# Kernel tuning notes

Measured on AMD Instinct MI355X. Metric: run time of the kernel, lower is better.

The kernel has to match this reference:

```python
import jax, jax.numpy as jnp
import numpy as np

N = 256   # num_atoms
V = 64    # v_dim
E = 64    # e_dim
S = 16    # num_sims
H = 16    # hidden size hard-coded in the module


def setup_inputs() -> dict:
    key = jax.random.key(0)
    ks = jax.random.split(key, 12)
    # edge index lists equivalent to the one-hot rel_rec / rel_send matmuls
    off_diag = np.ones((N, N), dtype=np.float32) - np.eye(N, dtype=np.float32)
    send_np, recv_np = np.where(off_diag)  # rows=senders ([0]), cols=receivers ([1])
    def w(k, shape):
        fan_in = shape[0]
        return (jax.random.normal(k, shape, jnp.float32) / np.sqrt(fan_in)).astype(jnp.float32)
    return {
        "t": jnp.zeros((), jnp.float32),
        "v0": jax.random.normal(ks[0], (S, N, V), jnp.float32),
        "e0": jax.random.normal(ks[1], (S, N, N - 1, E), jnp.float32),
        "wv1": w(ks[2], (E, H)), "bv1": jnp.zeros((H,), jnp.float32),
        "wv2": w(ks[3], (H, V)), "bv2": jnp.zeros((V,), jnp.float32),
        "we1": w(ks[4], (2 * V, H)), "be1": jnp.zeros((H,), jnp.float32),
        "we2": w(ks[5], (H, E)), "be2": jnp.zeros((E,), jnp.float32),
        "recv_idx": jnp.asarray(recv_np, jnp.int32),
        "send_idx": jnp.asarray(send_np, jnp.int32),
    }


def reference(t, v0, e0, wv1, bv1, wv2, bv2, we1, be1, we2, be2, recv_idx, send_idx):
    # dv = mlp_v(sum_j e0[:, :, j, :])  -> [S, N, V]
    ev = jnp.sum(e0, axis=2)                               # [S, N, E]
    dv = jnp.tanh(ev @ wv1 + bv1) @ wv2 + bv2              # [S, N, V]

    # node2edge: one-hot matmuls == gathers along the node axis
    receivers = v0[:, recv_idx, :]                          # [S, N*(N-1), V]
    senders = v0[:, send_idx, :]                            # [S, N*(N-1), V]
    edges = jnp.concatenate([receivers, senders], axis=-1)  # [S, N*(N-1), 2V]

    de = jnp.tanh(edges @ we1 + be1) @ we2 + be2            # [S, N*(N-1), E]
    de = de.reshape(de.shape[0], N, N - 1, de.shape[-1])    # [S, N, N-1, E]
    return (dv, de)
```

## Files before the change

### kernel.cpp

```cpp
#include <hip/hip_runtime.h>
#include <cstddef>

#define NN 256
#define VD 64
#define ED 64
#define SD 16
#define HD 16
#define EPS 65280

__device__ __forceinline__ float fast_tanh(float x) {
    float e = __expf(2.0f * x);
    float r = __builtin_amdgcn_rcpf(e + 1.0f);
    return 1.0f - 2.0f * r;
}

__global__ __launch_bounds__(256) void precompute_ab(
    const float* __restrict__ v0, const float* __restrict__ we1,
    float* __restrict__ a_tab, float* __restrict__ b_tab) {
    int t = threadIdx.x;
    int i = t & 15;
    int nl = t >> 4;
    int node = blockIdx.x * 16 + nl;
    const float* vrow = v0 + (size_t)node * VD;
    float a = 0.f, b = 0.f;
    #pragma unroll
    for (int k = 0; k < VD; ++k) {
        float x = vrow[k];
        a += x * we1[k * HD + i];
        b += x * we1[(VD + k) * HD + i];
    }
    a_tab[node * HD + i] = a;
    b_tab[node * HD + i] = b;
}

__global__ __launch_bounds__(256) void dv_kernel(
    const float* __restrict__ e0,
    const float* __restrict__ wv1, const float* __restrict__ bv1,
    const float* __restrict__ wv2, const float* __restrict__ bv2,
    float* __restrict__ dv_out) {
    __shared__ float red[1024];
    __shared__ float ev_s[64];
    __shared__ float h_s[16];
    int t = threadIdx.x;
    int node = blockIdx.x;
    const float* base = e0 + (size_t)node * 255 * ED;
    int c = t & 15;
    int g = t >> 4;
    float4 acc = make_float4(0.f, 0.f, 0.f, 0.f);
    for (int j = g; j < 255; j += 16) {
        const float4 v = *(const float4*)(base + (size_t)j * ED + c * 4);
        acc.x += v.x; acc.y += v.y; acc.z += v.z; acc.w += v.w;
    }
    *(float4*)(red + g * 64 + c * 4) = acc;
    __syncthreads();
    if (t < 64) {
        float s = 0.f;
        #pragma unroll
        for (int gg = 0; gg < 16; ++gg) s += red[gg * 64 + t];
        ev_s[t] = s;
    }
    __syncthreads();
    if (t < 16) {
        float ah = bv1[t];
        #pragma unroll
        for (int e = 0; e < 64; ++e) ah += ev_s[e] * wv1[e * HD + t];
        h_s[t] = fast_tanh(ah);
    }
    __syncthreads();
    if (t < 64) {
        float o = bv2[t];
        #pragma unroll
        for (int i = 0; i < HD; ++i) o += h_s[i] * wv2[i * VD + t];
        dv_out[(size_t)node * VD + t] = o;
    }
}

__global__ __launch_bounds__(256) void de_kernel(
    const float* __restrict__ a_tab, const float* __restrict__ b_tab,
    const float* __restrict__ we2, const float* __restrict__ be1,
    const float* __restrict__ be2,
    const int* __restrict__ recv_idx, const int* __restrict__ send_idx,
    float* __restrict__ de_out) {
    __shared__ float h_s[64 * 20];
    int t = threadIdx.x;
    int s = blockIdx.y;
    int tile = blockIdx.x;
    int p = t & 63;
    int iq = t >> 6;
    int eg = tile * 64 + p;

    int r  = recv_idx[eg];
    int sd = send_idx[eg];
    const float4 av = *(const float4*)(a_tab + ((s << 8) + r)  * HD + iq * 4);
    const float4 bv = *(const float4*)(b_tab + ((s << 8) + sd) * HD + iq * 4);
    const float4 b1 = *(const float4*)(be1 + iq * 4);
    float4 hv;
    hv.x = fast_tanh(av.x + bv.x + b1.x);
    hv.y = fast_tanh(av.y + bv.y + b1.y);
    hv.z = fast_tanh(av.z + bv.z + b1.z);
    hv.w = fast_tanh(av.w + bv.w + b1.w);
    *(float4*)(h_s + p * 20 + iq * 4) = hv;

    int v = t & 63;
    float w2[16];
    #pragma unroll
    for (int i = 0; i < HD; ++i) w2[i] = we2[i * ED + v];
    float bias = be2[v];
    __syncthreads();

    int w = t >> 6;
    size_t outbase = ((size_t)s * EPS + (size_t)tile * 64) * ED;
    for (int pp = w * 16; pp < w * 16 + 16; ++pp) {
        const float* hp = h_s + pp * 20;
        float o = bias;
        #pragma unroll
        for (int i = 0; i < HD; i += 4) {
            float4 h4 = *(const float4*)(hp + i);
            o += h4.x * w2[i] + h4.y * w2[i + 1] + h4.z * w2[i + 2] + h4.w * w2[i + 3];
        }
        de_out[outbase + (size_t)pp * ED + v] = o;
    }
}

extern "C" void kernel_launch(void* const* d_in, const int* in_sizes, int n_in,
                              void* d_out, int out_size, void* d_ws, size_t ws_size,
                              hipStream_t stream) {
    const float* v0   = (const float*)d_in[1];
    const float* e0   = (const float*)d_in[2];
    const float* wv1  = (const float*)d_in[3];
    const float* bv1  = (const float*)d_in[4];
    const float* wv2  = (const float*)d_in[5];
    const float* bv2  = (const float*)d_in[6];
    const float* we1  = (const float*)d_in[7];
    const float* be1  = (const float*)d_in[8];
    const float* we2  = (const float*)d_in[9];
    const float* be2  = (const float*)d_in[10];
    const int* recv_idx = (const int*)d_in[11];
    const int* send_idx = (const int*)d_in[12];

    float* dv_out = (float*)d_out;
    float* de_out = dv_out + (size_t)SD * NN * VD;
    float* a_tab  = (float*)d_ws;
    float* b_tab  = a_tab + 4096 * HD;

    precompute_ab<<<256, 256, 0, stream>>>(v0, we1, a_tab, b_tab);
    dv_kernel<<<SD * NN, 256, 0, stream>>>(e0, wv1, bv1, wv2, bv2, dv_out);
    de_kernel<<<dim3(EPS / 64, SD), 256, 0, stream>>>(a_tab, b_tab, we2, be1, be2,
                                                      recv_idx, send_idx, de_out);
}
```

Measured before the change: 497.6 us.

## Fuse dv and de kernels into one interleaved launch

Merges the read-heavy dv reduction kernel and the write-heavy de MLP kernel into a single launch. Every fifth block runs dv work and the other four run de tiles, so loads of e0 and stores of de_out proceed at the same time across the GPU. This aims to overlap the two memory-bound phases and remove one kernel launch. The price is branch divergence at block level, a shared-memory footprint sized for the larger of the two paths, and extra index arithmetic per block.

Measured after the change: 461.5 us. 7.3% less time.

```diff
diff --git a/kernel.cpp b/kernel.cpp
--- a/kernel.cpp
+++ b/kernel.cpp
@@ -7,6 +7,8 @@
 #define SD 16
 #define HD 16
 #define EPS 65280
+#define DE_TILES 16320
+#define DV_BLOCKS 4096
 
 __device__ __forceinline__ float fast_tanh(float x) {
     float e = __expf(2.0f * x);
@@ -33,92 +35,98 @@
     b_tab[node * HD + i] = b;
 }
 
-__global__ __launch_bounds__(256) void dv_kernel(
+__global__ __launch_bounds__(256) void fused_dv_de(
     const float* __restrict__ e0,
     const float* __restrict__ wv1, const float* __restrict__ bv1,
     const float* __restrict__ wv2, const float* __restrict__ bv2,
-    float* __restrict__ dv_out) {
-    __shared__ float red[1024];
-    __shared__ float ev_s[64];
-    __shared__ float h_s[16];
-    int t = threadIdx.x;
-    int node = blockIdx.x;
-    const float* base = e0 + (size_t)node * 255 * ED;
-    int c = t & 15;
-    int g = t >> 4;
-    float4 acc = make_float4(0.f, 0.f, 0.f, 0.f);
-    for (int j = g; j < 255; j += 16) {
-        const float4 v = *(const float4*)(base + (size_t)j * ED + c * 4);
-        acc.x += v.x; acc.y += v.y; acc.z += v.z; acc.w += v.w;
-    }
-    *(float4*)(red + g * 64 + c * 4) = acc;
-    __syncthreads();
-    if (t < 64) {
-        float s = 0.f;
-        #pragma unroll
-        for (int gg = 0; gg < 16; ++gg) s += red[gg * 64 + t];
-        ev_s[t] = s;
-    }
-    __syncthreads();
-    if (t < 16) {
-        float ah = bv1[t];
-        #pragma unroll
-        for (int e = 0; e < 64; ++e) ah += ev_s[e] * wv1[e * HD + t];
-        h_s[t] = fast_tanh(ah);
-    }
-    __syncthreads();
-    if (t < 64) {
-        float o = bv2[t];
-        #pragma unroll
-        for (int i = 0; i < HD; ++i) o += h_s[i] * wv2[i * VD + t];
-        dv_out[(size_t)node * VD + t] = o;
-    }
-}
-
-__global__ __launch_bounds__(256) void de_kernel(
     const float* __restrict__ a_tab, const float* __restrict__ b_tab,
     const float* __restrict__ we2, const float* __restrict__ be1,
     const float* __restrict__ be2,
     const int* __restrict__ recv_idx, const int* __restrict__ send_idx,
-    float* __restrict__ de_out) {
-    __shared__ float h_s[64 * 20];
+    float* __restrict__ dv_out, float* __restrict__ de_out) {
+    __shared__ float smem[1344];
+    int bid = blockIdx.x;
+    int q = bid / 5;
+    int r = bid - q * 5;
     int t = threadIdx.x;
-    int s = blockIdx.y;
-    int tile = blockIdx.x;
-    int p = t & 63;
-    int iq = t >> 6;
-    int eg = tile * 64 + p;
 
-    int r  = recv_idx[eg];
-    int sd = send_idx[eg];
-    const float4 av = *(const float4*)(a_tab + ((s << 8) + r)  * HD + iq * 4);
-    const float4 bv = *(const float4*)(b_tab + ((s << 8) + sd) * HD + iq * 4);
-    const float4 b1 = *(const float4*)(be1 + iq * 4);
-    float4 hv;
-    hv.x = fast_tanh(av.x + bv.x + b1.x);
-    hv.y = fast_tanh(av.y + bv.y + b1.y);
-    hv.z = fast_tanh(av.z + bv.z + b1.z);
-    hv.w = fast_tanh(av.w + bv.w + b1.w);
-    *(float4*)(h_s + p * 20 + iq * 4) = hv;
+    if (r == 4) {
+        float* red  = smem;
+        float* ev_s = smem + 1024;
+        float* h_s  = smem + 1088;
+        int node = q;
+        const float* base = e0 + (size_t)node * 255 * ED;
+        int c = t & 15;
+        int g = t >> 4;
+        float4 acc = make_float4(0.f, 0.f, 0.f, 0.f);
+        for (int j = g; j < 255; j += 16) {
+            const float4 v = *(const float4*)(base + (size_t)j * ED + c * 4);
+            acc.x += v.x; acc.y += v.y; acc.z += v.z; acc.w += v.w;
+        }
+        *(float4*)(red + g * 64 + c * 4) = acc;
+        __syncthreads();
+        if (t < 64) {
+            float s = 0.f;
+            #pragma unroll
+            for (int gg = 0; gg < 16; ++gg) s += red[gg * 64 + t];
+            ev_s[t] = s;
+        }
+        __syncthreads();
+        if (t < 16) {
+            float ah = bv1[t];
+            #pragma unroll
+            for (int e = 0; e < 64; ++e) ah += ev_s[e] * wv1[e * HD + t];
+            h_s[t] = fast_tanh(ah);
+        }
+        __syncthreads();
+        if (t < 64) {
+            float o = bv2[t];
+            #pragma unroll
+            for (int i = 0; i < HD; ++i) o += h_s[i] * wv2[i * VD + t];
+            dv_out[(size_t)node * VD + t] = o;
+        }
+    } else {
+        int dt = q * 4 + r;
+        if (dt >= DE_TILES) return;
+        int s = dt / 1020;
+        int tile = dt - s * 1020;
+        float* h_s = smem;
 
-    int v = t & 63;
-    float w2[16];
-    #pragma unroll
-    for (int i = 0; i < HD; ++i) w2[i] = we2[i * ED + v];
-    float bias = be2[v];
-    __syncthreads();
+        int p = t & 63;
+        int iq = t >> 6;
+        int eg = tile * 64 + p;
 
-    int w = t >> 6;
-    size_t outbase = ((size_t)s * EPS + (size_t)tile * 64) * ED;
-    for (int pp = w * 16; pp < w * 16 + 16; ++pp) {
-        const float* hp = h_s + pp * 20;
-        float o = bias;
+        int rr = recv_idx[eg];
+        int sd = send_idx[eg];
+        const float4 av = *(const float4*)(a_tab + ((s << 8) + rr) * HD + iq * 4);
+        const float4 bv = *(const float4*)(b_tab + ((s << 8) + sd) * HD + iq * 4);
+        const float4 b1 = *(const float4*)(be1 + iq * 4);
+        float4 hv;
+        hv.x = fast_tanh(av.x + bv.x + b1.x);
+        hv.y = fast_tanh(av.y + bv.y + b1.y);
+        hv.z = fast_tanh(av.z + bv.z + b1.z);
+        hv.w = fast_tanh(av.w + bv.w + b1.w);
+        *(float4*)(h_s + p * 20 + iq * 4) = hv;
+
+        int v = t & 63;
+        float w2[16];
         #pragma unroll
-        for (int i = 0; i < HD; i += 4) {
-            float4 h4 = *(const float4*)(hp + i);
-            o += h4.x * w2[i] + h4.y * w2[i + 1] + h4.z * w2[i + 2] + h4.w * w2[i + 3];
+        for (int i = 0; i < HD; ++i) w2[i] = we2[i * ED + v];
+        float bias = be2[v];
+        __syncthreads();
+
+        int w = t >> 6;
+        size_t outbase = ((size_t)s * EPS + (size_t)tile * 64) * ED;
+        for (int pp = w * 16; pp < w * 16 + 16; ++pp) {
+            const float* hp = h_s + pp * 20;
+            float o = bias;
+            #pragma unroll
+            for (int i = 0; i < HD; i += 4) {
+                float4 h4 = *(const float4*)(hp + i);
+                o += h4.x * w2[i] + h4.y * w2[i + 1] + h4.z * w2[i + 2] + h4.w * w2[i + 3];
+            }
+            de_out[outbase + (size_t)pp * ED + v] = o;
         }
-        de_out[outbase + (size_t)pp * ED + v] = o;
     }
 }
 
@@ -144,7 +152,7 @@
     float* b_tab  = a_tab + 4096 * HD;
 
     precompute_ab<<<256, 256, 0, stream>>>(v0, we1, a_tab, b_tab);
-    dv_kernel<<<SD * NN, 256, 0, stream>>>(e0, wv1, bv1, wv2, bv2, dv_out);
-    de_kernel<<<dim3(EPS / 64, SD), 256, 0, stream>>>(a_tab, b_tab, we2, be1, be2,
-                                                      recv_idx, send_idx, de_out);
+    fused_dv_de<<<DV_BLOCKS * 5, 256, 0, stream>>>(
+        e0, wv1, bv1, wv2, bv2, a_tab, b_tab, we2, be1, be2,
+        recv_idx, send_idx, dv_out, de_out);
 }
```
